# Kernel tuning notes

Hardware: AMD Instinct MI355X
Metric: run time of the kernel (lower is better)

The kernel has to match this reference:

```python
import jax, jax.numpy as jnp
import numpy as np

N_NODES = 100000


def _gcn_layer(x, src, dst, W, b, n):
    # PyG GCNConv: x' = x @ W, then symmetric-normalized aggregation with
    # self-loops (fill value 1), then + bias.
    h = x @ W  # [n, out]
    loop = jnp.arange(n, dtype=src.dtype)
    s = jnp.concatenate([src, loop])  # sources incl. self-loops
    d = jnp.concatenate([dst, loop])  # destinations incl. self-loops
    # degree computed on destination (col) with unit edge weights
    deg = jax.ops.segment_sum(jnp.ones_like(d, dtype=h.dtype), d, num_segments=n)
    dinv = jnp.where(deg > 0, jax.lax.rsqrt(deg), 0.0)
    norm = dinv[s] * dinv[d]  # [E+n]
    msg = h[s] * norm[:, None]  # gather + scale, [E+n, out]
    out = jax.ops.segment_sum(msg, d, num_segments=n)  # scatter-add
    return out + b


def setup_inputs() -> dict:
    key = jax.random.key(0)
    k1, k2, k3, k4, k5, k6 = jax.random.split(key, 6)
    in_c, hid_c, out_c = 5, 128, 64
    E = 1600000
    x = jax.random.normal(k1, (N_NODES, in_c), dtype=jnp.float32)
    edge_index = jax.random.randint(k2, (2, E), 0, N_NODES, dtype=jnp.int64)
    # Glorot-style init like PyG's Linear
    W1 = jax.random.normal(k3, (in_c, hid_c), dtype=jnp.float32) / np.sqrt(in_c)
    b1 = jnp.zeros((hid_c,), dtype=jnp.float32)
    W2 = jax.random.normal(k4, (hid_c, out_c), dtype=jnp.float32) / np.sqrt(hid_c)
    b2 = jnp.zeros((out_c,), dtype=jnp.float32)
    return {"x": x, "edge_index": edge_index, "W1": W1, "b1": b1, "W2": W2, "b2": b2}


def reference(x, edge_index, W1, b1, W2, b2):
    src, dst = edge_index[0], edge_index[1]
    n = x.shape[0]
    h = _gcn_layer(x, src, dst, W1, b1, n)
    h = jax.nn.relu(h)
    out = _gcn_layer(h, src, dst, W2, b2, n)
    return out
```

## Files before the change

### kernel.cpp

```cpp
#include <hip/hip_runtime.h>
#include <hip/hip_fp16.h>

#define IN_C 5
#define HID  128
#define OUTC 64

#define NBUCK_MAX 512
#define BCAP      4800
#define BIN_GRID  512
#define BIN_PER   3328
#define BIN_ITERS 13

typedef _Float16 f16x8 __attribute__((ext_vector_type(8)));
typedef float    f32x4 __attribute__((ext_vector_type(4)));

__global__ void __launch_bounds__(256)
k_init(const float* __restrict__ W2, __half* __restrict__ W2p,
       int* __restrict__ bucket_cnt) {
    if (blockIdx.x < 2) bucket_cnt[blockIdx.x * 256 + threadIdx.x] = 0;
    int i = blockIdx.x * 256 + threadIdx.x;
    int j = i & 7;
    int lane = (i >> 3) & 63;
    int kk = (i >> 9) & 3;
    int nt = i >> 11;
    int k = kk * 32 + (lane >> 4) * 8 + j;
    int nn = nt * 16 + (lane & 15);
    W2p[i] = __float2half(W2[k * OUTC + nn]);
}

__global__ void __launch_bounds__(256)
k_bin(const int* __restrict__ src, const int* __restrict__ dst,
      int* __restrict__ bucket_cnt, unsigned* __restrict__ binned, int E) {
    __shared__ int hist[NBUCK_MAX], base[NBUCK_MAX], lstart[NBUCK_MAX], cur[NBUCK_MAX];
    __shared__ unsigned staged[BIN_PER];
    __shared__ unsigned short sbuck[BIN_PER];
    int t = threadIdx.x;
    hist[t] = 0; hist[t + 256] = 0;
    __syncthreads();
    int per = (E + gridDim.x - 1) / gridDim.x;
    int lo = blockIdx.x * per, hi = min(E, lo + per);
    int ds[BIN_ITERS], ss[BIN_ITERS];
#pragma unroll
    for (int i = 0; i < BIN_ITERS; ++i) {
        int e = lo + t + i * 256;
        if (e < hi) {
            int d = dst[e];
            ds[i] = d; ss[i] = src[e];
            atomicAdd(&hist[d >> 8], 1);
        } else ds[i] = -1;
    }
    __syncthreads();
    if (hist[t] > 0)       base[t] = atomicAdd(&bucket_cnt[t], hist[t]);
    if (hist[t + 256] > 0) base[t + 256] = atomicAdd(&bucket_cnt[t + 256], hist[t + 256]);
    lstart[t] = hist[t]; lstart[t + 256] = hist[t + 256];
    __syncthreads();
#pragma unroll
    for (int off = 1; off < NBUCK_MAX; off <<= 1) {
        int a0 = (t >= off) ? lstart[t - off] : 0;
        int a1 = (t + 256 >= off) ? lstart[t + 256 - off] : 0;
        __syncthreads();
        lstart[t] += a0; lstart[t + 256] += a1;
        __syncthreads();
    }
    {
        int e0 = lstart[t] - hist[t];
        int e1 = lstart[t + 256] - hist[t + 256];
        __syncthreads();
        lstart[t] = e0; lstart[t + 256] = e1;
        cur[t] = e0; cur[t + 256] = e1;
    }
    __syncthreads();
#pragma unroll
    for (int i = 0; i < BIN_ITERS; ++i) {
        if (ds[i] >= 0) {
            int d = ds[i];
            int b = d >> 8;
            int pos = atomicAdd(&cur[b], 1);
            staged[pos] = ((unsigned)ss[i] << 8) | (unsigned)(d & 255);
            sbuck[pos] = (unsigned short)b;
        }
    }
    __syncthreads();
    int mtot = hi - lo;
    for (int s = t; s < mtot; s += 256) {
        int b = sbuck[s];
        binned[(size_t)b * BCAP + base[b] + (s - lstart[b])] = staged[s];
    }
}

__global__ void __launch_bounds__(256)
k_csr(const unsigned* __restrict__ binned, const int* __restrict__ bucket_cnt,
      const float* __restrict__ x,
      int* __restrict__ rowptr, int* __restrict__ cnt, float* __restrict__ dinv,
      __half* __restrict__ xs, int* __restrict__ col, int n, int nb) {
    __shared__ int sc[NBUCK_MAX];
    __shared__ int hist[256], sc2[256], cur[256];
    __shared__ int staged[BCAP];
    int b = blockIdx.x;
    int t = threadIdx.x;

    sc[t]       = (t < nb) ? bucket_cnt[t] : 0;
    sc[t + 256] = (t + 256 < nb) ? bucket_cnt[t + 256] : 0;
    __syncthreads();
#pragma unroll
    for (int off = 1; off < NBUCK_MAX; off <<= 1) {
        int a0 = (t >= off) ? sc[t - off] : 0;
        int a1 = (t + 256 >= off) ? sc[t + 256 - off] : 0;
        __syncthreads();
        sc[t] += a0; sc[t + 256] += a1;
        __syncthreads();
    }
    int m = bucket_cnt[b];
    int ebase = (b == 0) ? 0 : sc[b - 1];
    const unsigned* bin = binned + (size_t)b * BCAP;

    hist[t] = 0;
    __syncthreads();
    for (int e = t; e < m; e += 256)
        atomicAdd(&hist[bin[e] & 255], 1);
    __syncthreads();

    int h = hist[t];
    sc2[t] = h;
    __syncthreads();
#pragma unroll
    for (int off = 1; off < 256; off <<= 1) {
        int a = (t >= off) ? sc2[t - off] : 0;
        __syncthreads();
        sc2[t] += a;
        __syncthreads();
    }
    int rs = sc2[t] - h;
    cur[t] = rs;

    int v = b * 256 + t;
    if (v < n) {
        rowptr[v] = ebase + rs;
        cnt[v] = h;
        float dv = rsqrtf(1.0f + (float)h);
        dinv[v] = dv;
        const float* xp = x + (size_t)v * IN_C;
        __half2 hh[4];
        hh[0] = __floats2half2_rn(xp[0] * dv, xp[1] * dv);
        hh[1] = __floats2half2_rn(xp[2] * dv, xp[3] * dv);
        hh[2] = __floats2half2_rn(xp[4] * dv, 0.f);
        hh[3] = __floats2half2_rn(0.f, 0.f);
        *(uint4*)(xs + (size_t)v * 8) = *(uint4*)hh;
    }
    __syncthreads();
    for (int e = t; e < m; e += 256) {
        unsigned p = bin[e];
        int pos = atomicAdd(&cur[p & 255], 1);
        staged[pos] = (int)(p >> 8);
    }
    __syncthreads();
    for (int e = t; e < m; e += 256)
        col[ebase + e] = staged[e];
}

#define NB 64
#define H1STRIDE 132
__global__ void __launch_bounds__(256, 7)
k_fused(const __half* __restrict__ xs, const float* __restrict__ dinv,
        const int* __restrict__ rowptr, const int* __restrict__ cnt,
        const int* __restrict__ col,
        const float* __restrict__ W1, const float* __restrict__ b1,
        const __half* __restrict__ W2p, __half* __restrict__ g2, int n) {
    __shared__ __half sh_h1[NB * H1STRIDE];
    __shared__ float sh_xa[NB * 9];
    __shared__ float sh_dinv[NB];
    __shared__ int sh_start[NB], sh_len[NB];
    __shared__ __half2 sh_w1[IN_C * 64];
    __shared__ float sh_b1[HID];
    int t = threadIdx.x;
    int base = blockIdx.x * NB;

    for (int idx = t; idx < IN_C * 64; idx += 256) {
        int k = idx >> 6, jp = idx & 63;
        float2 w = *(const float2*)(W1 + k * HID + 2 * jp);
        sh_w1[idx] = __floats2half2_rn(w.x, w.y);
    }
    if (t < HID) sh_b1[t] = b1[t];

    if (t < NB) {
        int v = base + t;
        if (v < n) {
            sh_start[t] = rowptr[v];
            sh_len[t]   = cnt[v];
            sh_dinv[t]  = dinv[v];
        } else {
            sh_start[t] = 0; sh_len[t] = 0; sh_dinv[t] = 0.f;
        }
    }
    __syncthreads();

    {
        int q = t & 7;
#pragma unroll
        for (int half = 0; half < 2; ++half) {
            int vl = (t >> 3) + half * 32;
            int v = base + vl;
            int start = sh_start[vl], len = sh_len[vl];
            float a0 = 0.f, a1 = 0.f, a2 = 0.f, a3 = 0.f, a4 = 0.f;
            if (q == 0 && v < n) {
                uint4 r = *(const uint4*)(xs + (size_t)v * 8);
                const __half2* h = (const __half2*)&r;
                float2 f0 = __half22float2(h[0]), f1 = __half22float2(h[1]), f2 = __half22float2(h[2]);
                a0 = f0.x; a1 = f0.y; a2 = f1.x; a3 = f1.y; a4 = f2.x;
            }
            for (int k = q; k < len; k += 8) {
                int s = col[start + k];
                uint4 r = *(const uint4*)(xs + (size_t)s * 8);
                const __half2* h = (const __half2*)&r;
                float2 f0 = __half22float2(h[0]), f1 = __half22float2(h[1]), f2 = __half22float2(h[2]);
                a0 += f0.x; a1 += f0.y; a2 += f1.x; a3 += f1.y; a4 += f2.x;
            }
#pragma unroll
            for (int d = 1; d <= 4; d <<= 1) {
                a0 += __shfl_down(a0, d, 64);
                a1 += __shfl_down(a1, d, 64);
                a2 += __shfl_down(a2, d, 64);
                a3 += __shfl_down(a3, d, 64);
                a4 += __shfl_down(a4, d, 64);
            }
            if (q == 0) {
                float* sx = sh_xa + vl * 9;
                sx[0] = a0; sx[1] = a1; sx[2] = a2; sx[3] = a3; sx[4] = a4;
            }
        }
    }
    __syncthreads();

    {
        int v = t >> 2;
        const float* xa = sh_xa + v * 9;
        float x0 = xa[0], x1 = xa[1], x2 = xa[2], x3 = xa[3], x4 = xa[4];
        float dv = sh_dinv[v];
        __half* hrow = sh_h1 + v * H1STRIDE;
#pragma unroll
        for (int i = 0; i < 16; ++i) {
            int jp = (t & 3) + 4 * i;
            float2 w0 = __half22float2(sh_w1[jp]);
            float2 w1v = __half22float2(sh_w1[64 + jp]);
            float2 w2v = __half22float2(sh_w1[128 + jp]);
            float2 w3 = __half22float2(sh_w1[192 + jp]);
            float2 w4 = __half22float2(sh_w1[256 + jp]);
            float acc0 = x0 * w0.x + x1 * w1v.x + x2 * w2v.x + x3 * w3.x + x4 * w4.x;
            float acc1 = x0 * w0.y + x1 * w1v.y + x2 * w2v.y + x3 * w3.y + x4 * w4.y;
            int j0 = jp * 2;
            float2 bb = *(const float2*)(sh_b1 + j0);
            *(__half2*)(hrow + j0) =
                __floats2half2_rn(fmaxf(acc0 * dv + bb.x, 0.f), fmaxf(acc1 * dv + bb.y, 0.f));
        }
    }
    __syncthreads();

    {
        int w = t >> 6;
        int lane = t & 63;
        int quad = lane >> 4, nn = lane & 15;
        const __half* arow = sh_h1 + (size_t)(w * 16 + nn) * H1STRIDE + quad * 8;
        f16x8 afr[4];
#pragma unroll
        for (int kk = 0; kk < 4; ++kk)
            afr[kk] = *(const f16x8*)(arow + kk * 32);

        const f16x8* bp = (const f16x8*)W2p + lane;
#pragma unroll
        for (int nt = 0; nt < 4; ++nt) {
            f32x4 acc = {0.f, 0.f, 0.f, 0.f};
#pragma unroll
            for (int kk = 0; kk < 4; ++kk)
                acc = __builtin_amdgcn_mfma_f32_16x16x32_f16(
                    afr[kk], bp[(nt * 4 + kk) * 64], acc, 0, 0, 0);
#pragma unroll
            for (int r = 0; r < 4; ++r) {
                int vl = w * 16 + quad * 4 + r;
                int v = base + vl;
                if (v < n)
                    g2[(size_t)v * OUTC + nt * 16 + nn] =
                        __float2half(acc[r] * sh_dinv[vl]);
            }
        }
    }
}

__global__ void __launch_bounds__(256)
k_agg2(const __half* __restrict__ g2, const float* __restrict__ dinv,
       const int* __restrict__ rowptr, const int* __restrict__ cnt,
       const int* __restrict__ col, const float* __restrict__ b2,
       float* __restrict__ out, int n) {
    int t = threadIdx.x;
    int v = blockIdx.x * 4 + (t >> 6);
    if (v >= n) return;
    int lane = t & 63;
    int slot = lane >> 3;
    int oct  = lane & 7;
    int start = rowptr[v], len = cnt[v];
    float a0 = 0.f, a1 = 0.f, a2 = 0.f, a3 = 0.f, a4 = 0.f, a5 = 0.f, a6 = 0.f, a7 = 0.f;
    int it = slot;
    for (; it + 8 < len; it += 16) {
        int s0 = col[start + it];
        int s1 = col[start + it + 8];
        uint4 r0 = *(const uint4*)(g2 + (size_t)s0 * OUTC + oct * 8);
        uint4 r1 = *(const uint4*)(g2 + (size_t)s1 * OUTC + oct * 8);
        const __half2* h0 = (const __half2*)&r0;
        const __half2* h1 = (const __half2*)&r1;
        float2 f0 = __half22float2(h0[0]), f1 = __half22float2(h0[1]);
        float2 f2 = __half22float2(h0[2]), f3 = __half22float2(h0[3]);
        float2 g0 = __half22float2(h1[0]), g1 = __half22float2(h1[1]);
        float2 g2v = __half22float2(h1[2]), g3 = __half22float2(h1[3]);
        a0 += f0.x + g0.x; a1 += f0.y + g0.y; a2 += f1.x + g1.x; a3 += f1.y + g1.y;
        a4 += f2.x + g2v.x; a5 += f2.y + g2v.y; a6 += f3.x + g3.x; a7 += f3.y + g3.y;
    }
    for (; it < len; it += 8) {
        int s = col[start + it];
        uint4 raw = *(const uint4*)(g2 + (size_t)s * OUTC + oct * 8);
        const __half2* h = (const __half2*)&raw;
        float2 f0 = __half22float2(h[0]), f1 = __half22float2(h[1]);
        float2 f2 = __half22float2(h[2]), f3 = __half22float2(h[3]);
        a0 += f0.x; a1 += f0.y; a2 += f1.x; a3 += f1.y;
        a4 += f2.x; a5 += f2.y; a6 += f3.x; a7 += f3.y;
    }
#pragma unroll
    for (int d = 8; d <= 32; d <<= 1) {
        a0 += __shfl_down(a0, d, 64); a1 += __shfl_down(a1, d, 64);
        a2 += __shfl_down(a2, d, 64); a3 += __shfl_down(a3, d, 64);
        a4 += __shfl_down(a4, d, 64); a5 += __shfl_down(a5, d, 64);
        a6 += __shfl_down(a6, d, 64); a7 += __shfl_down(a7, d, 64);
    }
    if (lane < 8) {
        uint4 raw = *(const uint4*)(g2 + (size_t)v * OUTC + oct * 8);
        const __half2* h = (const __half2*)&raw;
        float2 s0 = __half22float2(h[0]), s1 = __half22float2(h[1]);
        float2 s2 = __half22float2(h[2]), s3 = __half22float2(h[3]);
        const float4* bp = (const float4*)(b2 + oct * 8);
        float4 bb0 = bp[0], bb1 = bp[1];
        float dv = dinv[v];
        float4 o0 = make_float4(dv * (a0 + s0.x) + bb0.x,
                                dv * (a1 + s0.y) + bb0.y,
                                dv * (a2 + s1.x) + bb0.z,
                                dv * (a3 + s1.y) + bb0.w);
        float4 o1 = make_float4(dv * (a4 + s2.x) + bb1.x,
                                dv * (a5 + s2.y) + bb1.y,
                                dv * (a6 + s3.x) + bb1.z,
                                dv * (a7 + s3.y) + bb1.w);
        float4* op = (float4*)(out + (size_t)v * OUTC + oct * 8);
        op[0] = o0; op[1] = o1;
    }
}


extern "C" void kernel_launch(void* const* d_in, const int* in_sizes, int n_in,
                              void* d_out, int out_size, void* d_ws, size_t ws_size,
                              hipStream_t stream) {
    const float* x  = (const float*)d_in[0];
    const int*   ei = (const int*)d_in[1];
    const float* W1 = (const float*)d_in[2];
    const float* b1 = (const float*)d_in[3];
    const float* W2 = (const float*)d_in[4];
    const float* b2 = (const float*)d_in[5];
    float*       out = (float*)d_out;

    const int n = in_sizes[0] / IN_C;
    const int E = in_sizes[1] / 2;
    const int* src = ei;
    const int* dst = ei + E;
    const int nbuck = (n + 255) / 256;

    char* ws = (char*)d_ws;
    size_t off = 0;
    int* cnt         = (int*)(ws + off); off += (size_t)n * 4;
    int* rowptr      = (int*)(ws + off); off += (size_t)n * 4;
    int* col         = (int*)(ws + off); off += (size_t)E * 4;
    float* dinv      = (float*)(ws + off); off += (size_t)n * 4;
    __half* xs       = (__half*)(ws + off); off += (size_t)n * 8 * 2;
    __half* g2       = (__half*)(ws + off); off += (size_t)n * OUTC * 2;
    __half* W2p      = (__half*)(ws + off); off += (size_t)HID * OUTC * 2;
    int* bucket_cnt  = (int*)(ws + off); off += NBUCK_MAX * 4;
    unsigned* binned = (unsigned*)(ws + off); off += (size_t)NBUCK_MAX * BCAP * 4;

    const int B = 256;

    k_init<<<(HID * OUTC) / B, B, 0, stream>>>(W2, W2p, bucket_cnt);
    k_bin<<<BIN_GRID, B, 0, stream>>>(src, dst, bucket_cnt, binned, E);
    k_csr<<<nbuck, B, 0, stream>>>(binned, bucket_cnt, x,
                                   rowptr, cnt, dinv, xs, col, n, nbuck);

    k_fused<<<(n + NB - 1) / NB, B, 0, stream>>>(xs, dinv, rowptr, cnt, col,
                                                 W1, b1, W2p, g2, n);
    k_agg2<<<(n + 3) / 4, B, 0, stream>>>(g2, dinv, rowptr, cnt, col, b2, out, n);
}
```

Before: 179.0 us.

## Map 8 lanes per node in second aggregation and use fma_mix accumulation

The second-layer aggregation kernel now assigns 8 threads per destination node (32 nodes per block) instead of a full 64-lane wavefront per node. That removes the cross-slot shuffle reduction and the idle lanes in the epilogue, and every lane writes output. Half-to-float conversion and add are fused into inline v_fma_mix_f32 instructions, with two accumulator sets for ILP. In exchange, each thread walks the whole neighbor list serially, so load balance now depends on degree variance within a wavefront and fewer loads per node are in flight at once.

```diff
diff --git a/kernel.cpp b/kernel.cpp
--- a/kernel.cpp
+++ b/kernel.cpp
@@ -285,69 +285,80 @@
     }
 }
 
+
+#define MIX_LO(A, W) \
+    asm("v_fma_mix_f32 %0, %1, %2, %0 op_sel:[0,0,0] op_sel_hi:[1,0,0]" \
+        : "+v"(A) : "v"(W), "v"(one))
+#define MIX_HI(A, W) \
+    asm("v_fma_mix_f32 %0, %1, %2, %0 op_sel:[1,0,0] op_sel_hi:[1,0,0]" \
+        : "+v"(A) : "v"(W), "v"(one))
+
+#define ACC8(P, R)            \
+    do {                      \
+        MIX_LO(P##0, (R).x);  \
+        MIX_HI(P##1, (R).x);  \
+        MIX_LO(P##2, (R).y);  \
+        MIX_HI(P##3, (R).y);  \
+        MIX_LO(P##4, (R).z);  \
+        MIX_HI(P##5, (R).z);  \
+        MIX_LO(P##6, (R).w);  \
+        MIX_HI(P##7, (R).w);  \
+    } while (0)
+
 __global__ void __launch_bounds__(256)
 k_agg2(const __half* __restrict__ g2, const float* __restrict__ dinv,
        const int* __restrict__ rowptr, const int* __restrict__ cnt,
        const int* __restrict__ col, const float* __restrict__ b2,
        float* __restrict__ out, int n) {
     int t = threadIdx.x;
-    int v = blockIdx.x * 4 + (t >> 6);
+    int g = t >> 3;
+    int oct = t & 7;
+    int v = blockIdx.x * 32 + g;
     if (v >= n) return;
-    int lane = t & 63;
-    int slot = lane >> 3;
-    int oct  = lane & 7;
+
     int start = rowptr[v], len = cnt[v];
-    float a0 = 0.f, a1 = 0.f, a2 = 0.f, a3 = 0.f, a4 = 0.f, a5 = 0.f, a6 = 0.f, a7 = 0.f;
-    int it = slot;
-    for (; it + 8 < len; it += 16) {
+    float one = 1.0f;
+
+    float a0 = 0.f, a1 = 0.f, a2 = 0.f, a3 = 0.f,
+          a4 = 0.f, a5 = 0.f, a6 = 0.f, a7 = 0.f;
+    float c0 = 0.f, c1 = 0.f, c2 = 0.f, c3 = 0.f,
+          c4 = 0.f, c5 = 0.f, c6 = 0.f, c7 = 0.f;
+
+    int it = 0;
+    for (; it + 2 <= len; it += 2) {
         int s0 = col[start + it];
-        int s1 = col[start + it + 8];
-        uint4 r0 = *(const uint4*)(g2 + (size_t)s0 * OUTC + oct * 8);
-        uint4 r1 = *(const uint4*)(g2 + (size_t)s1 * OUTC + oct * 8);
-        const __half2* h0 = (const __half2*)&r0;
-        const __half2* h1 = (const __half2*)&r1;
-        float2 f0 = __half22float2(h0[0]), f1 = __half22float2(h0[1]);
-        float2 f2 = __half22float2(h0[2]), f3 = __half22float2(h0[3]);
-        float2 g0 = __half22float2(h1[0]), g1 = __half22float2(h1[1]);
-        float2 g2v = __half22float2(h1[2]), g3 = __half22float2(h1[3]);
-        a0 += f0.x + g0.x; a1 += f0.y + g0.y; a2 += f1.x + g1.x; a3 += f1.y + g1.y;
-        a4 += f2.x + g2v.x; a5 += f2.y + g2v.y; a6 += f3.x + g3.x; a7 += f3.y + g3.y;
-    }
-    for (; it < len; it += 8) {
-        int s = col[start + it];
-        uint4 raw = *(const uint4*)(g2 + (size_t)s * OUTC + oct * 8);
-        const __half2* h = (const __half2*)&raw;
-        float2 f0 = __half22float2(h[0]), f1 = __half22float2(h[1]);
-        float2 f2 = __half22float2(h[2]), f3 = __half22float2(h[3]);
-        a0 += f0.x; a1 += f0.y; a2 += f1.x; a3 += f1.y;
-        a4 += f2.x; a5 += f2.y; a6 += f3.x; a7 += f3.y;
-    }
-#pragma unroll
-    for (int d = 8; d <= 32; d <<= 1) {
-        a0 += __shfl_down(a0, d, 64); a1 += __shfl_down(a1, d, 64);
-        a2 += __shfl_down(a2, d, 64); a3 += __shfl_down(a3, d, 64);
-        a4 += __shfl_down(a4, d, 64); a5 += __shfl_down(a5, d, 64);
-        a6 += __shfl_down(a6, d, 64); a7 += __shfl_down(a7, d, 64);
-    }
-    if (lane < 8) {
-        uint4 raw = *(const uint4*)(g2 + (size_t)v * OUTC + oct * 8);
-        const __half2* h = (const __half2*)&raw;
-        float2 s0 = __half22float2(h[0]), s1 = __half22float2(h[1]);
-        float2 s2 = __half22float2(h[2]), s3 = __half22float2(h[3]);
-        const float4* bp = (const float4*)(b2 + oct * 8);
-        float4 bb0 = bp[0], bb1 = bp[1];
-        float dv = dinv[v];
-        float4 o0 = make_float4(dv * (a0 + s0.x) + bb0.x,
-                                dv * (a1 + s0.y) + bb0.y,
-                                dv * (a2 + s1.x) + bb0.z,
-                                dv * (a3 + s1.y) + bb0.w);
-        float4 o1 = make_float4(dv * (a4 + s2.x) + bb1.x,
-                                dv * (a5 + s2.y) + bb1.y,
-                                dv * (a6 + s3.x) + bb1.z,
-                                dv * (a7 + s3.y) + bb1.w);
-        float4* op = (float4*)(out + (size_t)v * OUTC + oct * 8);
-        op[0] = o0; op[1] = o1;
-    }
+        int s1 = col[start + it + 1];
+        uint4 r0 = *(const uint4*)(g2 + ((size_t)s0 << 6) + (oct << 3));
+        uint4 r1 = *(const uint4*)(g2 + ((size_t)s1 << 6) + (oct << 3));
+        ACC8(a, r0);
+        ACC8(c, r1);
+    }
+    if (it < len) {
+        int s0 = col[start + it];
+        uint4 r0 = *(const uint4*)(g2 + ((size_t)s0 << 6) + (oct << 3));
+        ACC8(a, r0);
+    }
+
+    {
+        uint4 rs = *(const uint4*)(g2 + ((size_t)v << 6) + (oct << 3));
+        ACC8(a, rs);
+    }
+
+    a0 += c0; a1 += c1; a2 += c2; a3 += c3;
+    a4 += c4; a5 += c5; a6 += c6; a7 += c7;
+
+    float dv = dinv[v];
+    const float* bp = b2 + (oct << 3);
+    float4 bb0 = *(const float4*)bp;
+    float4 bb1 = *(const float4*)(bp + 4);
+
+    float4 o0 = make_float4(dv * a0 + bb0.x, dv * a1 + bb0.y,
+                            dv * a2 + bb0.z, dv * a3 + bb0.w);
+    float4 o1 = make_float4(dv * a4 + bb1.x, dv * a5 + bb1.y,
+                            dv * a6 + bb1.z, dv * a7 + bb1.w);
+    float4* op = (float4*)(out + ((size_t)v << 6) + (oct << 3));
+    op[0] = o0;
+    op[1] = o1;
 }
 
 
@@ -389,5 +400,5 @@
 
     k_fused<<<(n + NB - 1) / NB, B, 0, stream>>>(xs, dinv, rowptr, cnt, col,
                                                  W1, b1, W2p, g2, n);
-    k_agg2<<<(n + 3) / 4, B, 0, stream>>>(g2, dinv, rowptr, cnt, col, b2, out, n);
-}
+    k_agg2<<<(n + 31) / 32, B, 0, stream>>>(g2, dinv, rowptr, cnt, col, b2, out, n);
+}
```

Result: faster. 171.8 us (-4.0%).
